# Kernel tuning notes

Hardware: AMD Instinct MI355X
Metric: run time of the kernel (lower is better)

Reference implementation:

```python
import jax, jax.numpy as jnp
import numpy as np

LN_EPS = 1e-5

def _layernorm(x, scale, bias):
    mu = jnp.mean(x, axis=-1, keepdims=True)
    var = jnp.var(x, axis=-1, keepdims=True)
    return (x - mu) * jax.lax.rsqrt(var + LN_EPS) * scale + bias

def setup_inputs() -> dict:
    T, node_num, num_nodes, E, C = 4, 10000, 50000, 256, 128
    key = jax.random.key(0)
    ks = jax.random.split(key, 12)
    s = lambda fan_in: 1.0 / np.sqrt(fan_in)
    return {
        "x": jax.random.normal(ks[0], (T * node_num, E), jnp.float32),
        "batched_x": jax.random.normal(ks[1], (num_nodes, E), jnp.float32),
        "indices": jax.random.randint(ks[2], (T, node_num), 0, num_nodes, jnp.int32),
        "ln_d_scale": jnp.ones((E,), jnp.float32),
        "ln_d_bias": jnp.zeros((E,), jnp.float32),
        "W1_d": jax.random.normal(ks[3], (E, 2 * E), jnp.float32) * s(E),
        "b1_d": jnp.zeros((2 * E,), jnp.float32),
        "W2_d": jax.random.normal(ks[4], (2 * E, C), jnp.float32) * s(2 * E),
        "b2_d": jnp.zeros((C,), jnp.float32),
        "ln_u_scale": jnp.ones((C,), jnp.float32),
        "ln_u_bias": jnp.zeros((C,), jnp.float32),
        "W1_u": jax.random.normal(ks[5], (C, 2 * C), jnp.float32) * s(C),
        "b1_u": jnp.zeros((2 * C,), jnp.float32),
        "W2_u": jax.random.normal(ks[6], (2 * C, E), jnp.float32) * s(2 * C),
        "b2_u": jnp.zeros((E,), jnp.float32),
    }

def reference(x, batched_x, indices, ln_d_scale, ln_d_bias, W1_d, b1_d, W2_d, b2_d,
              ln_u_scale, ln_u_bias, W1_u, b1_u, W2_u, b2_u):
    T, node_num = indices.shape
    num_nodes, E = batched_x.shape
    xr = x.reshape(T, node_num, E)
    # _to_entire: per-step scatter-add of active-node embeddings into the full node table
    def scatter_one(xi, idx):
        return jnp.zeros((num_nodes, E), x.dtype).at[idx].add(xi)
    ta = jax.vmap(scatter_one)(xr, indices)          # [T, num_nodes, E]
    inp = ta + batched_x[None]                        # broadcast entire features
    h = _layernorm(inp, ln_d_scale, ln_d_bias)
    h = jax.nn.gelu(h @ W1_d + b1_d, approximate=False) @ W2_d + b2_d  # [T, num_nodes, C]
    # _from_entire: gather each step's active nodes back, concat, LN + MLP up
    g = jnp.take_along_axis(h, indices[..., None], axis=1)  # [T, node_num, C]
    g = g.reshape(T * node_num, -1)
    g = _layernorm(g, ln_u_scale, ln_u_bias)
    out = jax.nn.gelu(g @ W1_u + b1_u, approximate=False) @ W2_u + b2_u  # [T*node_num, E]
    return out
```

## Files before the change

kernel.cpp:

```cpp
#include <hip/hip_runtime.h>
#include <math.h>

#define T_STEPS   4
#define NODE_NUM  10000
#define NUM_NODES 50000
#define E         256
#define TWO_E     512
#define CC        128
#define TWO_C     256
#define ROWS      32

typedef short bf16x8 __attribute__((ext_vector_type(8)));
typedef float f32x4  __attribute__((ext_vector_type(4)));
typedef unsigned short u16x4 __attribute__((ext_vector_type(4)));

#define MFMA16(a, b, c) __builtin_amdgcn_mfma_f32_16x16x32_bf16((a), (b), (c), 0, 0, 0)

static __device__ unsigned short g_wt[294912];
static __device__ int g_cnt[T_STEPS * NUM_NODES];
static __device__ int g_dup[T_STEPS * NODE_NUM];
static __device__ int g_ndup[T_STEPS];

__device__ __forceinline__ float geluf(float v) {
    return 0.5f * v * (1.0f + erff(v * 0.70710678118654752440f));
}

__device__ __forceinline__ unsigned short f2bf(float f) {
    unsigned int u = __builtin_bit_cast(unsigned int, f);
    u += 0x7fffu + ((u >> 16) & 1u);
    return (unsigned short)(u >> 16);
}

__global__ void prep_weights(const float* __restrict__ W1d, const float* __restrict__ W2d,
                             const float* __restrict__ W1u, const float* __restrict__ W2u) {
    int i = blockIdx.x * 256 + threadIdx.x;
    if (i < T_STEPS * NUM_NODES) g_cnt[i] = 0;
    if (i < T_STEPS) g_ndup[i] = 0;
    if (i < 131072) {
        int n = i >> 8, k = i & 255;
        g_wt[i] = f2bf(W1d[(size_t)k * TWO_E + n]);
    }
    if (i < 65536) {
        int n = i >> 9, k = i & 511;
        g_wt[131072 + i] = f2bf(W2d[(size_t)k * CC + n]);
    }
    if (i < 32768) {
        int n = i >> 7, k = i & 127;
        g_wt[196608 + i] = f2bf(W1u[(size_t)k * TWO_C + n]);
    }
    if (i < 65536) {
        int n = i >> 8, k = i & 255;
        g_wt[229376 + i] = f2bf(W2u[(size_t)k * E + n]);
    }
}

__global__ void count_kernel(const int* __restrict__ indices) {
    int gr = blockIdx.x * 256 + threadIdx.x;
    if (gr < T_STEPS * NODE_NUM) {
        int t = gr / NODE_NUM;
        atomicAdd(&g_cnt[t * NUM_NODES + indices[gr]], 1);
    }
}

__global__ void compact_zero_kernel(float* __restrict__ table,
                                    const int* __restrict__ indices,
                                    int gr0, int t0, int grLim, int slab) {
    int gr = gr0 + blockIdx.x * 256 + threadIdx.x;
    if (gr >= grLim) return;
    int t = gr / NODE_NUM;
    int idx = indices[gr];
    if (g_cnt[t * NUM_NODES + idx] < 2) return;
    int pos = atomicAdd(&g_ndup[slab], 1);
    g_dup[gr0 + pos] = gr;
    float4* rp = reinterpret_cast<float4*>(&table[((size_t)(t - t0) * NUM_NODES + idx) * E]);
    float4 z = make_float4(0.f, 0.f, 0.f, 0.f);
    #pragma unroll
    for (int k = 0; k < 64; ++k) rp[k] = z;
}

__global__ void scatter_list_kernel(float* __restrict__ table,
                                    const float* __restrict__ x,
                                    const int* __restrict__ indices,
                                    int gr0, int t0, int slab) {
    int nd = g_ndup[slab];
    for (int e = blockIdx.x; e < nd; e += gridDim.x) {
        int gr = g_dup[gr0 + e];
        int t = gr / NODE_NUM;
        int idx = indices[gr];
        atomicAdd(&table[((size_t)(t - t0) * NUM_NODES + idx) * E + threadIdx.x],
                  x[(size_t)gr * E + threadIdx.x]);
    }
}

__global__ __launch_bounds__(256, 3)
void mlp_kernel(const float* __restrict__ table,
                const float* __restrict__ x,
                const float* __restrict__ batched_x,
                const int* __restrict__ indices,
                const float* __restrict__ lnd_s, const float* __restrict__ lnd_b,
                const float* __restrict__ b1d, const float* __restrict__ b2d,
                const float* __restrict__ lnu_s, const float* __restrict__ lnu_b,
                const float* __restrict__ b1u, const float* __restrict__ b2u,
                float* __restrict__ out,
                int gr0, int t0, int grLim) {
    __shared__ __align__(16) unsigned char smem[33280];

    unsigned short* Xs  = (unsigned short*)smem;
    unsigned short* H1  = (unsigned short*)smem;
    float*          H2f = (float*)smem;
    unsigned short* H2b = (unsigned short*)(smem + 16896);
    unsigned short* G1  = (unsigned short*)smem;

    const unsigned short* w1t  = g_wt;
    const unsigned short* w2t  = g_wt + 131072;
    const unsigned short* w1ut = g_wt + 196608;
    const unsigned short* w2ut = g_wt + 229376;

    const int tid = threadIdx.x;
    const int w = tid >> 6, lane = tid & 63;
    const int l16 = lane & 15, quad = lane >> 4;
    const int grb = gr0 + blockIdx.x * ROWS;

    {
        const int c4 = lane * 4;
        const float4 sc = *reinterpret_cast<const float4*>(lnd_s + c4);
        const float4 bi = *reinterpret_cast<const float4*>(lnd_b + c4);
        #pragma unroll
        for (int it = 0; it < 8; ++it) {
            const int r = it * 4 + w;
            int gr = grb + r;
            if (gr >= grLim) gr = grLim - 1;
            const int t = gr / NODE_NUM;
            const int idx = indices[gr];
            const float* src = (g_cnt[t * NUM_NODES + idx] > 1)
                ? (table + ((size_t)(t - t0) * NUM_NODES + idx) * E)
                : (x + (size_t)gr * E);
            float4 a = *reinterpret_cast<const float4*>(src + c4);
            float4 b = *reinterpret_cast<const float4*>(batched_x + (size_t)idx * E + c4);
            a.x += b.x; a.y += b.y; a.z += b.z; a.w += b.w;
            float s  = a.x + a.y + a.z + a.w;
            float sq = a.x*a.x + a.y*a.y + a.z*a.z + a.w*a.w;
            #pragma unroll
            for (int m = 1; m < 64; m <<= 1) {
                s  += __shfl_xor(s,  m);
                sq += __shfl_xor(sq, m);
            }
            const float mu = s * (1.0f / E);
            const float rs = rsqrtf(sq * (1.0f / E) - mu * mu + 1e-5f);
            u16x4 o;
            o.x = f2bf((a.x - mu) * rs * sc.x + bi.x);
            o.y = f2bf((a.y - mu) * rs * sc.y + bi.y);
            o.z = f2bf((a.z - mu) * rs * sc.z + bi.z);
            o.w = f2bf((a.w - mu) * rs * sc.w + bi.w);
            *reinterpret_cast<u16x4*>(&Xs[r * 264 + c4]) = o;
        }
    }
    __syncthreads();

    {
        bf16x8 af[2][8];
        #pragma unroll
        for (int mt = 0; mt < 2; ++mt) {
            const unsigned short* base = Xs + (l16 + 16 * mt) * 264 + quad * 8;
            #pragma unroll
            for (int ks = 0; ks < 8; ++ks)
                af[mt][ks] = *reinterpret_cast<const bf16x8*>(base + ks * 32);
        }
        __syncthreads();
        #pragma unroll
        for (int nt_ = 0; nt_ < 8; ++nt_) {
            int n = (w * 8 + nt_) * 16 + l16;
            const unsigned short* bp = w1t + (size_t)n * 256 + quad * 8;
            f32x4 a0 = {0.f, 0.f, 0.f, 0.f}, a1 = {0.f, 0.f, 0.f, 0.f};
            #pragma unroll
            for (int ks = 0; ks < 8; ++ks) {
                bf16x8 b = *reinterpret_cast<const bf16x8*>(bp + ks * 32);
                a0 = MFMA16(af[0][ks], b, a0);
                a1 = MFMA16(af[1][ks], b, a1);
            }
            float bias = b1d[n];
            #pragma unroll
            for (int reg = 0; reg < 4; ++reg) {
                int r = quad * 4 + reg;
                H1[r * 520 + n]        = f2bf(geluf(a0[reg] + bias));
                H1[(r + 16) * 520 + n] = f2bf(geluf(a1[reg] + bias));
            }
        }
    }
    __syncthreads();

    {
        f32x4 acc2[2][2];
        #pragma unroll
        for (int i = 0; i < 2; ++i)
            #pragma unroll
            for (int j = 0; j < 2; ++j) acc2[i][j] = (f32x4){0.f, 0.f, 0.f, 0.f};
        bf16x8 af2[2][8];
        #pragma unroll
        for (int mt = 0; mt < 2; ++mt) {
            const unsigned short* base = H1 + (l16 + 16 * mt) * 520 + quad * 8;
            #pragma unroll
            for (int ks = 0; ks < 8; ++ks)
                af2[mt][ks] = *reinterpret_cast<const bf16x8*>(base + ks * 32);
        }
        #pragma unroll
        for (int nt2 = 0; nt2 < 2; ++nt2) {
            int n = (w * 2 + nt2) * 16 + l16;
            const unsigned short* bp = w2t + (size_t)n * 512 + quad * 8;
            #pragma unroll
            for (int ks = 0; ks < 8; ++ks) {
                bf16x8 b = *reinterpret_cast<const bf16x8*>(bp + ks * 32);
                acc2[nt2][0] = MFMA16(af2[0][ks], b, acc2[nt2][0]);
                acc2[nt2][1] = MFMA16(af2[1][ks], b, acc2[nt2][1]);
            }
        }
        #pragma unroll
        for (int mt = 0; mt < 2; ++mt) {
            const unsigned short* base = H1 + (l16 + 16 * mt) * 520 + 256 + quad * 8;
            #pragma unroll
            for (int ks = 0; ks < 8; ++ks)
                af2[mt][ks] = *reinterpret_cast<const bf16x8*>(base + ks * 32);
        }
        __syncthreads();
        #pragma unroll
        for (int nt2 = 0; nt2 < 2; ++nt2) {
            int n = (w * 2 + nt2) * 16 + l16;
            const unsigned short* bp = w2t + (size_t)n * 512 + 256 + quad * 8;
            #pragma unroll
            for (int ks = 0; ks < 8; ++ks) {
                bf16x8 b = *reinterpret_cast<const bf16x8*>(bp + ks * 32);
                acc2[nt2][0] = MFMA16(af2[0][ks], b, acc2[nt2][0]);
                acc2[nt2][1] = MFMA16(af2[1][ks], b, acc2[nt2][1]);
            }
        }
        #pragma unroll
        for (int nt2 = 0; nt2 < 2; ++nt2) {
            int n = (w * 2 + nt2) * 16 + l16;
            float bias = b2d[n];
            #pragma unroll
            for (int mt = 0; mt < 2; ++mt)
                #pragma unroll
                for (int reg = 0; reg < 4; ++reg) {
                    int r = mt * 16 + quad * 4 + reg;
                    H2f[r * 132 + n] = acc2[nt2][mt][reg] + bias;
                }
        }
    }
    __syncthreads();

    {
        int row = tid >> 3, l8 = tid & 7;
        float s = 0.f, sq = 0.f;
        #pragma unroll
        for (int k = 0; k < 16; ++k) {
            float v = H2f[row * 132 + k * 8 + l8];
            s += v; sq += v * v;
        }
        s  += __shfl_xor(s, 1);  s  += __shfl_xor(s, 2);  s  += __shfl_xor(s, 4);
        sq += __shfl_xor(sq, 1); sq += __shfl_xor(sq, 2); sq += __shfl_xor(sq, 4);
        float mu = s * (1.0f / CC);
        float var = sq * (1.0f / CC) - mu * mu;
        float rs = rsqrtf(var + 1e-5f);
        #pragma unroll
        for (int k = 0; k < 16; ++k) {
            int c = k * 8 + l8;
            float v = (H2f[row * 132 + c] - mu) * rs * lnu_s[c] + lnu_b[c];
            H2b[row * 136 + c] = f2bf(v);
        }
    }
    __syncthreads();

    {
        bf16x8 af3[2][4];
        #pragma unroll
        for (int mt = 0; mt < 2; ++mt) {
            const unsigned short* base = H2b + (l16 + 16 * mt) * 136 + quad * 8;
            #pragma unroll
            for (int ks = 0; ks < 4; ++ks)
                af3[mt][ks] = *reinterpret_cast<const bf16x8*>(base + ks * 32);
        }
        #pragma unroll
        for (int nt_ = 0; nt_ < 4; ++nt_) {
            int n = (w * 4 + nt_) * 16 + l16;
            const unsigned short* bp = w1ut + (size_t)n * 128 + quad * 8;
            f32x4 a0 = {0.f, 0.f, 0.f, 0.f}, a1 = {0.f, 0.f, 0.f, 0.f};
            #pragma unroll
            for (int ks = 0; ks < 4; ++ks) {
                bf16x8 b = *reinterpret_cast<const bf16x8*>(bp + ks * 32);
                a0 = MFMA16(af3[0][ks], b, a0);
                a1 = MFMA16(af3[1][ks], b, a1);
            }
            float bias = b1u[n];
            #pragma unroll
            for (int reg = 0; reg < 4; ++reg) {
                int r = quad * 4 + reg;
                G1[r * 264 + n]        = f2bf(geluf(a0[reg] + bias));
                G1[(r + 16) * 264 + n] = f2bf(geluf(a1[reg] + bias));
            }
        }
    }
    __syncthreads();

    {
        bf16x8 af4[2][8];
        #pragma unroll
        for (int mt = 0; mt < 2; ++mt) {
            const unsigned short* base = G1 + (l16 + 16 * mt) * 264 + quad * 8;
            #pragma unroll
            for (int ks = 0; ks < 8; ++ks)
                af4[mt][ks] = *reinterpret_cast<const bf16x8*>(base + ks * 32);
        }
        #pragma unroll
        for (int nt_ = 0; nt_ < 4; ++nt_) {
            int n = (w * 4 + nt_) * 16 + l16;
            const unsigned short* bp = w2ut + (size_t)n * 256 + quad * 8;
            f32x4 a0 = {0.f, 0.f, 0.f, 0.f}, a1 = {0.f, 0.f, 0.f, 0.f};
            #pragma unroll
            for (int ks = 0; ks < 8; ++ks) {
                bf16x8 b = *reinterpret_cast<const bf16x8*>(bp + ks * 32);
                a0 = MFMA16(af4[0][ks], b, a0);
                a1 = MFMA16(af4[1][ks], b, a1);
            }
            float bias = b2u[n];
            #pragma unroll
            for (int reg = 0; reg < 4; ++reg) {
                int r = quad * 4 + reg;
                int g0 = grb + r, g1 = grb + r + 16;
                if (g0 < grLim) out[(size_t)g0 * E + n] = a0[reg] + bias;
                if (g1 < grLim) out[(size_t)g1 * E + n] = a1[reg] + bias;
            }
        }
    }
}

extern "C" void kernel_launch(void* const* d_in, const int* in_sizes, int n_in,
                              void* d_out, int out_size, void* d_ws, size_t ws_size,
                              hipStream_t stream) {
    const float* x     = (const float*)d_in[0];
    const float* bx    = (const float*)d_in[1];
    const int*   idxp  = (const int*)  d_in[2];
    const float* lnd_s = (const float*)d_in[3];
    const float* lnd_b = (const float*)d_in[4];
    const float* W1d   = (const float*)d_in[5];
    const float* b1d   = (const float*)d_in[6];
    const float* W2d   = (const float*)d_in[7];
    const float* b2d   = (const float*)d_in[8];
    const float* lnu_s = (const float*)d_in[9];
    const float* lnu_b = (const float*)d_in[10];
    const float* W1u   = (const float*)d_in[11];
    const float* b1u   = (const float*)d_in[12];
    const float* W2u   = (const float*)d_in[13];
    const float* b2u   = (const float*)d_in[14];
    float* out = (float*)d_out;
    float* table = (float*)d_ws;

    const size_t slice_bytes = (size_t)NUM_NODES * E * sizeof(float);
    int tb = (int)(ws_size / slice_bytes);
    if (tb < 1) tb = 1;
    if (tb > T_STEPS) tb = T_STEPS;

    prep_weights<<<784, 256, 0, stream>>>(W1d, W2d, W1u, W2u);
    count_kernel<<<(T_STEPS * NODE_NUM + 255) / 256, 256, 0, stream>>>(idxp);

    for (int t0 = 0; t0 < T_STEPS; t0 += tb) {
        int tcur = T_STEPS - t0 < tb ? T_STEPS - t0 : tb;
        int nrows = tcur * NODE_NUM;
        int gr0 = t0 * NODE_NUM;
        int grLim = gr0 + nrows;
        int slab = t0 / tb;
        compact_zero_kernel<<<(nrows + 255) / 256, 256, 0, stream>>>(
            table, idxp, gr0, t0, grLim, slab);
        scatter_list_kernel<<<1024, E, 0, stream>>>(table, x, idxp, gr0, t0, slab);
        mlp_kernel<<<(nrows + ROWS - 1) / ROWS, 256, 0, stream>>>(
            table, x, bx, idxp, lnd_s, lnd_b, b1d, b2d,
            lnu_s, lnu_b, b1u, b2u, out, gr0, t0, grLim);
    }
}
```

Before: 289.1 us.

## Split hidden dim into two halves, fuse GEMM1/GEMM2 per half, approximate GELU

```diff
diff --git a/kernel.cpp b/kernel.cpp
--- a/kernel.cpp
+++ b/kernel.cpp
@@ -22,7 +22,8 @@
 static __device__ int g_ndup[T_STEPS];
 
 __device__ __forceinline__ float geluf(float v) {
-    return 0.5f * v * (1.0f + erff(v * 0.70710678118654752440f));
+    float p = v * (1.5957691216057308f + 0.07135481282636226f * v * v);
+    return v / (1.0f + __expf(-p));
 }
 
 __device__ __forceinline__ unsigned short f2bf(float f) {
@@ -92,7 +93,7 @@
     }
 }
 
-__global__ __launch_bounds__(256, 3)
+__global__ __launch_bounds__(256, 4)
 void mlp_kernel(const float* __restrict__ table,
                 const float* __restrict__ x,
                 const float* __restrict__ batched_x,
@@ -103,10 +104,10 @@
                 const float* __restrict__ b1u, const float* __restrict__ b2u,
                 float* __restrict__ out,
                 int gr0, int t0, int grLim) {
-    __shared__ __align__(16) unsigned char smem[33280];
+    __shared__ __align__(16) unsigned char smem[33792];
 
     unsigned short* Xs  = (unsigned short*)smem;
-    unsigned short* H1  = (unsigned short*)smem;
+    unsigned short* H1a = (unsigned short*)(smem + 16896);
     float*          H2f = (float*)smem;
     unsigned short* H2b = (unsigned short*)(smem + 16896);
     unsigned short* G1  = (unsigned short*)smem;
@@ -157,96 +158,83 @@
     }
     __syncthreads();
 
-    {
-        bf16x8 af[2][8];
-        #pragma unroll
-        for (int mt = 0; mt < 2; ++mt) {
-            const unsigned short* base = Xs + (l16 + 16 * mt) * 264 + quad * 8;
-            #pragma unroll
-            for (int ks = 0; ks < 8; ++ks)
-                af[mt][ks] = *reinterpret_cast<const bf16x8*>(base + ks * 32);
+    f32x4 acc2[2][2];
+    #pragma unroll
+    for (int i = 0; i < 2; ++i)
+        #pragma unroll
+        for (int j = 0; j < 2; ++j) acc2[i][j] = (f32x4){0.f, 0.f, 0.f, 0.f};
+
+    #pragma unroll
+    for (int s = 0; s < 2; ++s) {
+        {
+            bf16x8 af[2][8];
+            #pragma unroll
+            for (int mt = 0; mt < 2; ++mt) {
+                const unsigned short* base = Xs + (l16 + 16 * mt) * 264 + quad * 8;
+                #pragma unroll
+                for (int ks = 0; ks < 8; ++ks)
+                    af[mt][ks] = *reinterpret_cast<const bf16x8*>(base + ks * 32);
+            }
+            #pragma unroll
+            for (int nt_ = 0; nt_ < 4; ++nt_) {
+                int nl = w * 64 + nt_ * 16 + l16;
+                int ng = s * 256 + nl;
+                const unsigned short* bp = w1t + (size_t)ng * 256 + quad * 8;
+                f32x4 a0 = {0.f, 0.f, 0.f, 0.f}, a1 = {0.f, 0.f, 0.f, 0.f};
+                #pragma unroll
+                for (int ks = 0; ks < 8; ++ks) {
+                    bf16x8 b = *reinterpret_cast<const bf16x8*>(bp + ks * 32);
+                    a0 = MFMA16(af[0][ks], b, a0);
+                    a1 = MFMA16(af[1][ks], b, a1);
+                }
+                float bias = b1d[ng];
+                #pragma unroll
+                for (int reg = 0; reg < 4; ++reg) {
+                    int r = quad * 4 + reg;
+                    H1a[r * 264 + nl]        = f2bf(geluf(a0[reg] + bias));
+                    H1a[(r + 16) * 264 + nl] = f2bf(geluf(a1[reg] + bias));
+                }
+            }
         }
         __syncthreads();
-        #pragma unroll
-        for (int nt_ = 0; nt_ < 8; ++nt_) {
-            int n = (w * 8 + nt_) * 16 + l16;
-            const unsigned short* bp = w1t + (size_t)n * 256 + quad * 8;
-            f32x4 a0 = {0.f, 0.f, 0.f, 0.f}, a1 = {0.f, 0.f, 0.f, 0.f};
-            #pragma unroll
-            for (int ks = 0; ks < 8; ++ks) {
-                bf16x8 b = *reinterpret_cast<const bf16x8*>(bp + ks * 32);
-                a0 = MFMA16(af[0][ks], b, a0);
-                a1 = MFMA16(af[1][ks], b, a1);
-            }
-            float bias = b1d[n];
-            #pragma unroll
-            for (int reg = 0; reg < 4; ++reg) {
-                int r = quad * 4 + reg;
-                H1[r * 520 + n]        = f2bf(geluf(a0[reg] + bias));
-                H1[(r + 16) * 520 + n] = f2bf(geluf(a1[reg] + bias));
-            }
-        }
-    }
-    __syncthreads();
-
-    {
-        f32x4 acc2[2][2];
-        #pragma unroll
-        for (int i = 0; i < 2; ++i)
-            #pragma unroll
-            for (int j = 0; j < 2; ++j) acc2[i][j] = (f32x4){0.f, 0.f, 0.f, 0.f};
-        bf16x8 af2[2][8];
-        #pragma unroll
-        for (int mt = 0; mt < 2; ++mt) {
-            const unsigned short* base = H1 + (l16 + 16 * mt) * 520 + quad * 8;
-            #pragma unroll
-            for (int ks = 0; ks < 8; ++ks)
-                af2[mt][ks] = *reinterpret_cast<const bf16x8*>(base + ks * 32);
-        }
-        #pragma unroll
-        for (int nt2 = 0; nt2 < 2; ++nt2) {
-            int n = (w * 2 + nt2) * 16 + l16;
-            const unsigned short* bp = w2t + (size_t)n * 512 + quad * 8;
-            #pragma unroll
-            for (int ks = 0; ks < 8; ++ks) {
-                bf16x8 b = *reinterpret_cast<const bf16x8*>(bp + ks * 32);
-                acc2[nt2][0] = MFMA16(af2[0][ks], b, acc2[nt2][0]);
-                acc2[nt2][1] = MFMA16(af2[1][ks], b, acc2[nt2][1]);
-            }
-        }
-        #pragma unroll
-        for (int mt = 0; mt < 2; ++mt) {
-            const unsigned short* base = H1 + (l16 + 16 * mt) * 520 + 256 + quad * 8;
-            #pragma unroll
-            for (int ks = 0; ks < 8; ++ks)
-                af2[mt][ks] = *reinterpret_cast<const bf16x8*>(base + ks * 32);
+
+        {
+            bf16x8 afk[2][8];
+            #pragma unroll
+            for (int mt = 0; mt < 2; ++mt) {
+                const unsigned short* base = H1a + (l16 + 16 * mt) * 264 + quad * 8;
+                #pragma unroll
+                for (int ks = 0; ks < 8; ++ks)
+                    afk[mt][ks] = *reinterpret_cast<const bf16x8*>(base + ks * 32);
+            }
+            #pragma unroll
+            for (int nt2 = 0; nt2 < 2; ++nt2) {
+                int n2 = (w * 2 + nt2) * 16 + l16;
+                const unsigned short* bp = w2t + (size_t)n2 * 512 + s * 256 + quad * 8;
+                #pragma unroll
+                for (int ks = 0; ks < 8; ++ks) {
+                    bf16x8 b = *reinterpret_cast<const bf16x8*>(bp + ks * 32);
+                    acc2[nt2][0] = MFMA16(afk[0][ks], b, acc2[nt2][0]);
+                    acc2[nt2][1] = MFMA16(afk[1][ks], b, acc2[nt2][1]);
+                }
+            }
+            if (s == 1) {
+                #pragma unroll
+                for (int nt2 = 0; nt2 < 2; ++nt2) {
+                    int n2 = (w * 2 + nt2) * 16 + l16;
+                    float bias = b2d[n2];
+                    #pragma unroll
+                    for (int mt = 0; mt < 2; ++mt)
+                        #pragma unroll
+                        for (int reg = 0; reg < 4; ++reg) {
+                            int r = mt * 16 + quad * 4 + reg;
+                            H2f[r * 132 + n2] = acc2[nt2][mt][reg] + bias;
+                        }
+                }
+            }
         }
         __syncthreads();
-        #pragma unroll
-        for (int nt2 = 0; nt2 < 2; ++nt2) {
-            int n = (w * 2 + nt2) * 16 + l16;
-            const unsigned short* bp = w2t + (size_t)n * 512 + 256 + quad * 8;
-            #pragma unroll
-            for (int ks = 0; ks < 8; ++ks) {
-                bf16x8 b = *reinterpret_cast<const bf16x8*>(bp + ks * 32);
-                acc2[nt2][0] = MFMA16(af2[0][ks], b, acc2[nt2][0]);
-                acc2[nt2][1] = MFMA16(af2[1][ks], b, acc2[nt2][1]);
-            }
-        }
-        #pragma unroll
-        for (int nt2 = 0; nt2 < 2; ++nt2) {
-            int n = (w * 2 + nt2) * 16 + l16;
-            float bias = b2d[n];
-            #pragma unroll
-            for (int mt = 0; mt < 2; ++mt)
-                #pragma unroll
-                for (int reg = 0; reg < 4; ++reg) {
-                    int r = mt * 16 + quad * 4 + reg;
-                    H2f[r * 132 + n] = acc2[nt2][mt][reg] + bias;
-                }
-        }
-    }
-    __syncthreads();
+    }
 
     {
         int row = tid >> 3, l8 = tid & 7;
```

After: 302.9 us. 1.05x slower.
